# Kernel optimization log

Hardware: AMD Instinct MI355X
Metric: run time of the kernel (lower is better)

Reference implementation:

```python
import jax, jax.numpy as jnp
import numpy as np

NUM_HEADS = 16
DEPTH = 0


def rotate_half(x):
    x1, x2 = jnp.split(x, 2, axis=-1)
    return jnp.concatenate((-x2, x1), axis=-1)


def rotary_tables(seq_len, rot_dim, dtype):
    # RotaryEmbedding(dim=rot_dim): inv_freq over even indices of rot_dim
    inv_freq = 1.0 / (10000.0 ** (jnp.arange(0, rot_dim, 2, dtype=jnp.float32) / rot_dim))
    freqs = jnp.arange(seq_len, dtype=jnp.float32)[:, None] * inv_freq[None, :]  # [N, rot_dim/2]
    emb = jnp.concatenate((freqs, freqs), axis=-1)  # [N, rot_dim]
    return emb.astype(dtype), jnp.cos(emb).astype(dtype), jnp.sin(emb).astype(dtype)


def setup_inputs() -> dict:
    key = jax.random.key(0)
    ks = jax.random.split(key, 7)
    B, N, C = 1, 2048, 1024
    hd = C // NUM_HEADS
    std_qkv = (1.0 / C) ** 0.5
    std_proj = (1.0 / (2 * C)) ** 0.5
    return {
        "x": jax.random.normal(ks[0], (B, N, C), dtype=jnp.float32),
        "W_qkv": jax.random.normal(ks[1], (6 * C, C), dtype=jnp.float32) * std_qkv,
        "W_proj": jax.random.normal(ks[2], (C, 2 * C), dtype=jnp.float32) * std_proj,
        "lambda_q1": jax.random.normal(ks[3], (hd,), dtype=jnp.float32) * 0.1,
        "lambda_q2": jax.random.normal(ks[4], (hd,), dtype=jnp.float32) * 0.1,
        "lambda_k1": jax.random.normal(ks[5], (hd,), dtype=jnp.float32) * 0.1,
        "lambda_k2": jax.random.normal(ks[6], (hd,), dtype=jnp.float32) * 0.1,
    }


def reference(x, W_qkv, W_proj, lambda_q1, lambda_q2, lambda_k1, lambda_k2):
    B, N, C = x.shape
    H = NUM_HEADS
    hd = C // H
    scale = hd ** -0.5
    lambda_init = 0.8 - 0.6 * np.exp(-0.3 * DEPTH)

    qkv = jnp.einsum('bnc,dc->bnd', x, W_qkv)               # [B,N,6C]
    qkv = qkv.reshape(B, N, 6, H, hd).transpose(2, 0, 3, 1, 4)  # [6,B,H,N,hd]
    q = jnp.concatenate((qkv[0], qkv[1]), axis=-1)          # [B,H,N,2hd]
    k = jnp.concatenate((qkv[2], qkv[3]), axis=-1)
    v = jnp.concatenate((qkv[4], qkv[5]), axis=-1)

    _, cos, sin = rotary_tables(N, 2 * hd, x.dtype)          # [N,2hd]
    q = q * cos + rotate_half(q) * sin
    k = k * cos + rotate_half(k) * sin

    q1, q2 = jnp.split(q, 2, axis=-1)                        # [B,H,N,hd] each
    k1, k2 = jnp.split(k, 2, axis=-1)

    attn1 = jnp.einsum('bhid,bhjd->bhij', q1, k1) * scale
    attn2 = jnp.einsum('bhid,bhjd->bhij', q2, k2) * scale

    lam1 = jnp.exp(jnp.sum(lambda_q1 * lambda_k1))
    lam2 = jnp.exp(jnp.sum(lambda_q2 * lambda_k2))
    lam = (lam1 - lam2 + lambda_init).astype(x.dtype)

    probs = jax.nn.softmax(attn1, axis=-1) - lam * jax.nn.softmax(attn2, axis=-1)
    out = jnp.einsum('bhij,bhjd->bhid', probs, v)            # [B,H,N,2hd]
    out = out.transpose(0, 2, 1, 3).reshape(B, N, 2 * C)
    out = jnp.einsum('bnd,cd->bnc', out, W_proj)             # [B,N,C]
    return out
```

## Files before the change

### kernel.cpp

```cpp
#include <hip/hip_runtime.h>

using bf16_t = __bf16;
typedef __bf16 bf16x4 __attribute__((ext_vector_type(4)));
typedef __bf16 bf16x8 __attribute__((ext_vector_type(8)));
typedef float floatx4 __attribute__((ext_vector_type(4)));

#define MFMA_BF16(a, b, c) __builtin_amdgcn_mfma_f32_16x16x32_bf16((a), (b), (c), 0, 0, 0)

__device__ __forceinline__ void async_ld16(bf16_t* lds_dst, const bf16_t* g_src) {
    __builtin_amdgcn_global_load_lds(
        (const __attribute__((address_space(1))) void*)g_src,
        (__attribute__((address_space(3))) void*)lds_dst, 16, 0, 0);
}

__global__ __launch_bounds__(256) void cast_all(const float* __restrict__ x,
                                                const float* __restrict__ Wqkv,
                                                const float* __restrict__ Wproj,
                                                const float* __restrict__ lq1,
                                                const float* __restrict__ lq2,
                                                const float* __restrict__ lk1,
                                                const float* __restrict__ lk2,
                                                bf16_t* __restrict__ xb,
                                                bf16_t* __restrict__ Wqkvb,
                                                bf16_t* __restrict__ Wprojb,
                                                float* __restrict__ lamp) {
    const int b = blockIdx.x;
    if (b == 5120) {
        int l = threadIdx.x;
        if (l < 64) {
            float p1 = lq1[l] * lk1[l];
            float p2 = lq2[l] * lk2[l];
            #pragma unroll
            for (int d = 1; d < 64; d <<= 1) {
                p1 += __shfl_xor(p1, d);
                p2 += __shfl_xor(p2, d);
            }
            if (l == 0) *lamp = expf(p1) - expf(p2) + 0.2f;
        }
        return;
    }
    const float* src;
    bf16_t* dst;
    size_t i;
    if (b < 1024)      { src = x;     dst = xb;     i = (size_t)b * 256 + threadIdx.x; }
    else if (b < 4096) { src = Wqkv;  dst = Wqkvb;  i = (size_t)(b - 1024) * 256 + threadIdx.x; }
    else               { src = Wproj; dst = Wprojb; i = (size_t)(b - 4096) * 256 + threadIdx.x; }
    const floatx4 a = *(const floatx4*)(src + i * 8);
    const floatx4 c = *(const floatx4*)(src + i * 8 + 4);
    bf16x8 r;
    r[0] = (bf16_t)a[0]; r[1] = (bf16_t)a[1]; r[2] = (bf16_t)a[2]; r[3] = (bf16_t)a[3];
    r[4] = (bf16_t)c[0]; r[5] = (bf16_t)c[1]; r[6] = (bf16_t)c[2]; r[7] = (bf16_t)c[3];
    *(bf16x8*)(dst + i * 8) = r;
}

template <int BM, int BN, int BK, bool QKV_EPI, typename TC>
__global__ __launch_bounds__(256) void gemm_bt(const bf16_t* __restrict__ A,
                                               const bf16_t* __restrict__ B,
                                               TC* __restrict__ C,
                                               bf16_t* __restrict__ Qb,
                                               bf16_t* __restrict__ Kb,
                                               bf16_t* __restrict__ Vt,
                                               int M, int N, int K) {
    constexpr int KC = BK / 32;
    constexpr int CH = BK / 8;
    __shared__ __align__(16) bf16_t As[BM * BK];
    __shared__ __align__(16) bf16_t Bs[BN * BK];
    const int t = threadIdx.x;
    const int lane = t & 63, wave = t >> 6;
    const int q4 = lane >> 4, m16 = lane & 15;
    const int mblk = blockIdx.y * BM, nblk = blockIdx.x * BN;
    const int wr = wave >> 1, wc = wave & 1;
    constexpr int WM = BM / 2, WN = BN / 2;
    constexpr int NI = WM / 16, NJ = WN / 16;
    constexpr int AR = BM * BK / 2048;
    constexpr int BR = BN * BK / 2048;

    floatx4 acc[NI][NJ] = {};

    for (int k0 = 0; k0 < K; k0 += BK) {
        __syncthreads();
        #pragma unroll
        for (int rr = 0; rr < AR; ++rr) {
            int f = rr * 256 + t;
            async_ld16(&As[f * 8], &A[(size_t)(mblk + f / CH) * K + k0 + (f % CH) * 8]);
        }
        #pragma unroll
        for (int rr = 0; rr < BR; ++rr) {
            int f = rr * 256 + t;
            async_ld16(&Bs[f * 8], &B[(size_t)(nblk + f / CH) * K + k0 + (f % CH) * 8]);
        }
        __syncthreads();

        bf16x8 a[NI][KC], b[NJ][KC];
        #pragma unroll
        for (int i = 0; i < NI; ++i)
            #pragma unroll
            for (int kk = 0; kk < KC; ++kk)
                a[i][kk] = *(const bf16x8*)&As[(wr * WM + i * 16 + m16) * BK + kk * 32 + q4 * 8];
        #pragma unroll
        for (int j = 0; j < NJ; ++j)
            #pragma unroll
            for (int kk = 0; kk < KC; ++kk)
                b[j][kk] = *(const bf16x8*)&Bs[(wc * WN + j * 16 + m16) * BK + kk * 32 + q4 * 8];
        #pragma unroll
        for (int i = 0; i < NI; ++i)
            #pragma unroll
            for (int j = 0; j < NJ; ++j)
                #pragma unroll
                for (int kk = 0; kk < KC; ++kk)
                    acc[i][j] = MFMA_BF16(a[i][kk], b[j][kk], acc[i][j]);
    }

    #pragma unroll
    for (int i = 0; i < NI; ++i)
        #pragma unroll
        for (int j = 0; j < NJ; ++j) {
            int n = nblk + wc * WN + j * 16 + m16;
            int mbase = mblk + wr * WM + i * 16 + q4 * 4;
            if constexpr (QKV_EPI) {
                int comp = n >> 10, h = (n >> 6) & 15, e = n & 63;
                if (comp < 2) {
                    #pragma unroll
                    for (int r = 0; r < 4; ++r)
                        Qb[(size_t)((comp * 16 + h) * 2048 + mbase + r) * 64 + e] =
                            (bf16_t)acc[i][j][r];
                } else if (comp < 4) {
                    #pragma unroll
                    for (int r = 0; r < 4; ++r)
                        Kb[(size_t)(((comp - 2) * 16 + h) * 2048 + mbase + r) * 64 + e] =
                            (bf16_t)acc[i][j][r];
                } else {
                    bf16x4 pv;
                    #pragma unroll
                    for (int r = 0; r < 4; ++r) pv[r] = (bf16_t)acc[i][j][r];
                    *(bf16x4*)&Vt[(size_t)(h * 128 + (comp - 4) * 64 + e) * 2048 + mbase] = pv;
                }
            } else {
                #pragma unroll
                for (int r = 0; r < 4; ++r)
                    C[(size_t)(mbase + r) * N + n] = (TC)acc[i][j][r];
            }
        }
}

__global__ __launch_bounds__(256) void rotary_inplace(bf16_t* __restrict__ Qb,
                                                      bf16_t* __restrict__ Kb) {
    int t = blockIdx.x * 256 + threadIdx.x;
    int e = t & 63, n = t >> 6;
    float invf = exp2f(-(float)e * (13.287712379549449f / 64.0f));
    float ang = (float)n * invf;
    float s, c;
    sincosf(ang, &s, &c);
    #pragma unroll 4
    for (int h = 0; h < 16; ++h) {
        int off = (h * 2048 + n) * 64 + e;
        float q1 = (float)Qb[off], q2 = (float)Qb[off + 2097152];
        Qb[off]           = (bf16_t)(q1 * c - q2 * s);
        Qb[off + 2097152] = (bf16_t)(q2 * c + q1 * s);
        float k1 = (float)Kb[off], k2 = (float)Kb[off + 2097152];
        Kb[off]           = (bf16_t)(k1 * c - k2 * s);
        Kb[off + 2097152] = (bf16_t)(k2 * c + k1 * s);
    }
}

__global__ __launch_bounds__(512, 4) void flash_diff(const bf16_t* __restrict__ Qb,
                                                     const bf16_t* __restrict__ Kb,
                                                     const bf16_t* __restrict__ Vt,
                                                     const float* __restrict__ lamp,
                                                     bf16_t* __restrict__ Ao) {
    constexpr int N = 2048, BN = 64, NT = N / BN;
    __shared__ __align__(16) bf16_t smem[40960];
    bf16_t* Pf = smem + 32768;
    const int t = threadIdx.x, lane = t & 63, w = t >> 6;
    const int comp = w >> 2, w4 = w & 3;
    const int q4 = lane >> 4, m16 = lane & 15;
    const int Lb = blockIdx.x;
    const int virt = (Lb & 7) * 64 + (Lb >> 3);
    const int h = virt >> 5, qt = virt & 31;
    const float lam = *lamp;
    const float cexp = 0.125f * 1.4426950408889634f;

    bf16x8 qf[2];
    const int qrow = qt * 64 + w4 * 16 + m16;
    #pragma unroll
    for (int kc = 0; kc < 2; ++kc)
        qf[kc] = *(const bf16x8*)&Qb[(size_t)((comp * 16 + h) * 2048 + qrow) * 64 + kc * 32 + q4 * 8];

    bf16x8 ones;
    #pragma unroll
    for (int j = 0; j < 8; ++j) ones[j] = (bf16_t)1.0f;

    floatx4 O[8] = {};
    floatx4 sm = {};

    auto stage = [&](bf16_t* Kd, bf16_t* Vd, int k0) {
        #pragma unroll
        for (int rr = 0; rr < 4; ++rr) {
            int idx = w * 4 + rr;
            if (idx < 16) {
                int i = idx >> 3, s = (idx >> 1) & 3, half = idx & 1;
                async_ld16(&Kd[idx * 512],
                           &Kb[(size_t)((i * 16 + h) * 2048 + k0 + 16 * s + m16) * 64 + half * 32 + q4 * 8]);
            } else {
                int v = idx - 16, tt = v >> 1, half = v & 1;
                async_ld16(&Vd[v * 512],
                           &Vt[(size_t)(h * 128 + tt * 16 + m16) * 2048 + k0 + half * 32 + q4 * 8]);
            }
        }
    };

    stage(smem, smem + 8192, 0);

    for (int it = 0; it < NT; ++it) {
        const int cur = it & 1;
        bf16_t* Kf = smem + cur * 16384;
        bf16_t* Vf = Kf + 8192;
        __syncthreads();
        if (it + 1 < NT) {
            bf16_t* Kn = smem + (cur ^ 1) * 16384;
            stage(Kn, Kn + 8192, (it + 1) * BN);
        }

        bf16_t* pw = &Pf[w * 1024];
        __builtin_amdgcn_s_setprio(1);
        #pragma unroll
        for (int s = 0; s < 4; ++s) {
            floatx4 sacc = {};
            const bf16x8 kf0 = *(const bf16x8*)&Kf[((comp * 4 + s) * 2 + 0) * 512 + lane * 8];
            const bf16x8 kf1 = *(const bf16x8*)&Kf[((comp * 4 + s) * 2 + 1) * 512 + lane * 8];
            sacc = MFMA_BF16(qf[0], kf0, sacc);
            sacc = MFMA_BF16(qf[1], kf1, sacc);
            __builtin_amdgcn_s_setprio(0);
            const int half = s >> 1, quad = (2 * s + (m16 >> 3)) & 3, jj = m16 & 7;
            #pragma unroll
            for (int r = 0; r < 4; ++r) {
                int u = quad * 16 + q4 * 4 + r;
                pw[half * 512 + (u ^ quad) * 8 + jj] = (bf16_t)exp2f(sacc[r] * cexp);
            }
            __builtin_amdgcn_s_setprio(1);
        }
        __builtin_amdgcn_s_setprio(0);

        bf16x8 pf[2];
        const int ur = lane ^ q4;
        pf[0] = *(const bf16x8*)&pw[0 * 512 + ur * 8];
        pf[1] = *(const bf16x8*)&pw[1 * 512 + ur * 8];
        sm = MFMA_BF16(pf[0], ones, sm);
        sm = MFMA_BF16(pf[1], ones, sm);
        __builtin_amdgcn_s_setprio(1);
        #pragma unroll
        for (int tt = 0; tt < 8; ++tt) {
            const bf16x8 vf0 = *(const bf16x8*)&Vf[(tt * 2 + 0) * 512 + lane * 8];
            const bf16x8 vf1 = *(const bf16x8*)&Vf[(tt * 2 + 1) * 512 + lane * 8];
            O[tt] = MFMA_BF16(pf[0], vf0, O[tt]);
            O[tt] = MFMA_BF16(pf[1], vf1, O[tt]);
        }
        __builtin_amdgcn_s_setprio(0);
    }

    float inv[4];
    #pragma unroll
    for (int r = 0; r < 4; ++r) inv[r] = 1.0f / sm[r];

    float* Ff = (float*)smem;
    __syncthreads();
    if (comp == 1) {
        #pragma unroll
        for (int tt = 0; tt < 8; ++tt) {
            floatx4 val;
            #pragma unroll
            for (int r = 0; r < 4; ++r) val[r] = lam * O[tt][r] * inv[r];
            *(floatx4*)&Ff[((w4 * 128 + tt * 16 + m16) << 4) + q4 * 4] = val;
        }
    }
    __syncthreads();
    if (comp == 0) {
        const int orow = qt * 64 + w4 * 16 + q4 * 4;
        #pragma unroll
        for (int tt = 0; tt < 8; ++tt) {
            const floatx4 v1 = *(const floatx4*)&Ff[((w4 * 128 + tt * 16 + m16) << 4) + q4 * 4];
            #pragma unroll
            for (int r = 0; r < 4; ++r) {
                float val = O[tt][r] * inv[r] - v1[r];
                Ao[(size_t)(orow + r) * 2048 + h * 128 + tt * 16 + m16] = (bf16_t)val;
            }
        }
    }
}

extern "C" void kernel_launch(void* const* d_in, const int* in_sizes, int n_in,
                              void* d_out, int out_size, void* d_ws, size_t ws_size,
                              hipStream_t stream) {
    const float* x     = (const float*)d_in[0];
    const float* Wqkv  = (const float*)d_in[1];
    const float* Wproj = (const float*)d_in[2];
    const float* lq1   = (const float*)d_in[3];
    const float* lq2   = (const float*)d_in[4];
    const float* lk1   = (const float*)d_in[5];
    const float* lk2   = (const float*)d_in[6];
    float* out = (float*)d_out;

    char* ws = (char*)d_ws;
    bf16_t* xb     = (bf16_t*)(ws);
    bf16_t* Ao     = (bf16_t*)(ws);
    bf16_t* Wqkvb  = (bf16_t*)(ws + 4194304);
    bf16_t* Wprojb = (bf16_t*)(ws + 16777216);
    bf16_t* Qb     = (bf16_t*)(ws + 20971520);
    bf16_t* Kb     = (bf16_t*)(ws + 29360128);
    bf16_t* Vt     = (bf16_t*)(ws + 37748736);
    float*  lamp   = (float*)(ws + 46137344);

    cast_all<<<5121, 256, 0, stream>>>(x, Wqkv, Wproj, lq1, lq2, lk1, lk2,
                                       xb, Wqkvb, Wprojb, lamp);
    gemm_bt<128, 128, 32, true, float><<<dim3(48, 16), 256, 0, stream>>>(
        xb, Wqkvb, (float*)nullptr, Qb, Kb, Vt, 2048, 6144, 1024);
    rotary_inplace<<<(2048 * 64) / 256, 256, 0, stream>>>(Qb, Kb);
    flash_diff<<<512, 512, 0, stream>>>(Qb, Kb, Vt, lamp, Ao);
    gemm_bt<64, 64, 64, false, float><<<dim3(16, 32), 256, 0, stream>>>(
        Ao, Wprojb, out, (bf16_t*)nullptr, (bf16_t*)nullptr, (bf16_t*)nullptr,
        2048, 1024, 2048);
}
```

Measured before the change: 240.4 us.

## Share P tiles across wave pairs to split the PV product 2x2

Each wave now reads the probability tiles written by two sibling waves through shared memory and computes the PV product for two 16-row query blocks over half of the V columns, instead of one query block over all columns. Each V fragment loaded from LDS is therefore reused across two MFMA row blocks, which halves V LDS reads per wave. This adds an extra barrier per KV tile so the P tiles are visible across waves, and it duplicates the row-sum MFMAs. The epilogue indexing is remapped to match the new ownership.

```diff
diff --git a/kernel.cpp b/kernel.cpp
--- a/kernel.cpp
+++ b/kernel.cpp
@@ -173,6 +173,7 @@
     bf16_t* Pf = smem + 32768;
     const int t = threadIdx.x, lane = t & 63, w = t >> 6;
     const int comp = w >> 2, w4 = w & 3;
+    const int aa = w4 >> 1, bb = w4 & 1;
     const int q4 = lane >> 4, m16 = lane & 15;
     const int Lb = blockIdx.x;
     const int virt = (Lb & 7) * 64 + (Lb >> 3);
@@ -190,8 +191,8 @@
     #pragma unroll
     for (int j = 0; j < 8; ++j) ones[j] = (bf16_t)1.0f;
 
-    floatx4 O[8] = {};
-    floatx4 sm = {};
+    floatx4 O[2][4] = {};
+    floatx4 sm[2] = {};
 
     auto stage = [&](bf16_t* Kd, bf16_t* Vd, int k0) {
         #pragma unroll
@@ -241,48 +242,66 @@
         }
         __builtin_amdgcn_s_setprio(0);
 
-        bf16x8 pf[2];
+        asm volatile("s_waitcnt lgkmcnt(0)" ::: "memory");
+        __builtin_amdgcn_s_barrier();
+
+        bf16x8 pf[2][2];
         const int ur = lane ^ q4;
-        pf[0] = *(const bf16x8*)&pw[0 * 512 + ur * 8];
-        pf[1] = *(const bf16x8*)&pw[1 * 512 + ur * 8];
-        sm = MFMA_BF16(pf[0], ones, sm);
-        sm = MFMA_BF16(pf[1], ones, sm);
+        #pragma unroll
+        for (int i = 0; i < 2; ++i) {
+            const int wsrc = comp * 4 + 2 * aa + i;
+            pf[i][0] = *(const bf16x8*)&Pf[wsrc * 1024 + 0 * 512 + ur * 8];
+            pf[i][1] = *(const bf16x8*)&Pf[wsrc * 1024 + 1 * 512 + ur * 8];
+            sm[i] = MFMA_BF16(pf[i][0], ones, sm[i]);
+            sm[i] = MFMA_BF16(pf[i][1], ones, sm[i]);
+        }
         __builtin_amdgcn_s_setprio(1);
         #pragma unroll
-        for (int tt = 0; tt < 8; ++tt) {
+        for (int v = 0; v < 4; ++v) {
+            const int tt = bb * 4 + v;
             const bf16x8 vf0 = *(const bf16x8*)&Vf[(tt * 2 + 0) * 512 + lane * 8];
             const bf16x8 vf1 = *(const bf16x8*)&Vf[(tt * 2 + 1) * 512 + lane * 8];
-            O[tt] = MFMA_BF16(pf[0], vf0, O[tt]);
-            O[tt] = MFMA_BF16(pf[1], vf1, O[tt]);
+            #pragma unroll
+            for (int i = 0; i < 2; ++i) {
+                O[i][v] = MFMA_BF16(pf[i][0], vf0, O[i][v]);
+                O[i][v] = MFMA_BF16(pf[i][1], vf1, O[i][v]);
+            }
         }
         __builtin_amdgcn_s_setprio(0);
     }
 
-    float inv[4];
+    float inv[2][4];
     #pragma unroll
-    for (int r = 0; r < 4; ++r) inv[r] = 1.0f / sm[r];
+    for (int i = 0; i < 2; ++i)
+        #pragma unroll
+        for (int r = 0; r < 4; ++r) inv[i][r] = 1.0f / sm[i][r];
 
     float* Ff = (float*)smem;
     __syncthreads();
     if (comp == 1) {
         #pragma unroll
-        for (int tt = 0; tt < 8; ++tt) {
-            floatx4 val;
-            #pragma unroll
-            for (int r = 0; r < 4; ++r) val[r] = lam * O[tt][r] * inv[r];
-            *(floatx4*)&Ff[((w4 * 128 + tt * 16 + m16) << 4) + q4 * 4] = val;
-        }
+        for (int i = 0; i < 2; ++i)
+            #pragma unroll
+            for (int v = 0; v < 4; ++v) {
+                floatx4 val;
+                #pragma unroll
+                for (int r = 0; r < 4; ++r) val[r] = lam * O[i][v][r] * inv[i][r];
+                *(floatx4*)&Ff[(((w4 * 2 + i) * 4 + v) * 16 + m16) * 16 + q4 * 4] = val;
+            }
     }
     __syncthreads();
     if (comp == 0) {
-        const int orow = qt * 64 + w4 * 16 + q4 * 4;
-        #pragma unroll
-        for (int tt = 0; tt < 8; ++tt) {
-            const floatx4 v1 = *(const floatx4*)&Ff[((w4 * 128 + tt * 16 + m16) << 4) + q4 * 4];
-            #pragma unroll
-            for (int r = 0; r < 4; ++r) {
-                float val = O[tt][r] * inv[r] - v1[r];
-                Ao[(size_t)(orow + r) * 2048 + h * 128 + tt * 16 + m16] = (bf16_t)val;
+        #pragma unroll
+        for (int i = 0; i < 2; ++i) {
+            const int orow = qt * 64 + (2 * aa + i) * 16 + q4 * 4;
+            #pragma unroll
+            for (int v = 0; v < 4; ++v) {
+                const floatx4 v1 = *(const floatx4*)&Ff[(((w4 * 2 + i) * 4 + v) * 16 + m16) * 16 + q4 * 4];
+                #pragma unroll
+                for (int r = 0; r < 4; ++r) {
+                    float val = O[i][v][r] * inv[i][r] - v1[r];
+                    Ao[(size_t)(orow + r) * 2048 + h * 128 + (bb * 4 + v) * 16 + m16] = (bf16_t)val;
+                }
             }
         }
     }
```

Result: no change. 240.9 us (+0.2%).
